# Optimization experiments

Hardware: AMD Instinct MI355X
Metric: run time of the kernel (lower is better)

## Reference

```python
import jax, jax.numpy as jnp
import numpy as np

TOP_K = 2


def setup_inputs() -> dict:
    key = jax.random.key(0)
    ks = jax.random.split(key, 4)
    T, E, D_IN, D_H, D_OUT = 8192, 8, 1024, 4096, 1024
    s_in = 1.0 / np.sqrt(D_IN)
    s_h = 1.0 / np.sqrt(D_H)
    return {
        "x": jax.random.normal(ks[0], (T, D_IN), dtype=jnp.float32),
        "Wg": jax.random.normal(ks[1], (D_IN, E), dtype=jnp.float32) * s_in,
        "bg": jnp.zeros((E,), dtype=jnp.float32),
        "W1": jax.random.normal(ks[2], (E, D_IN, D_H), dtype=jnp.float32) * s_in,
        "b1": jnp.zeros((E, D_H), dtype=jnp.float32),
        "W2": jax.random.normal(ks[3], (E, D_H, D_OUT), dtype=jnp.float32) * s_h,
        "b2": jnp.zeros((E, D_OUT), dtype=jnp.float32),
    }


def moe_forward(x, Wg, bg, W1, b1, W2, b2):
    # Top-k gate: logits [T,E] -> top-k -> softmax over the k selected logits,
    # scattered back into a dense [T,E] weight matrix (zeros elsewhere).
    logits = x @ Wg + bg                              # [T, E]
    topv, topi = jax.lax.top_k(logits, TOP_K)         # [T, k]
    topw = jax.nn.softmax(topv, axis=-1)              # [T, k]
    T, E = logits.shape
    weights = jnp.zeros((T, E), dtype=logits.dtype)
    rows = jnp.arange(T)[:, None]
    weights = weights.at[rows, topi].set(topw)        # dense gate weights [T, E]

    # Dense all-expert MLP (faithful to the naive torch module):
    h = jax.nn.relu(jnp.einsum("ti,eih->teh", x, W1) + b1[None])   # [T, E, H]
    expert_out = jnp.einsum("teh,eho->teo", h, W2) + b2[None]      # [T, E, O]

    # Top-k weighted sum over experts.
    return jnp.einsum("te,teo->to", weights, expert_out)           # [T, O]


def reference(x, Wg, bg, W1, b1, W2, b2):
    return moe_forward(x, Wg, bg, W1, b1, W2, b2)
```

## Files before the change

### kernel.cpp

```cpp
#include <hip/hip_runtime.h>
#include <hip/hip_bf16.h>
#include <stdint.h>

#define NTOK 8192
#define NE 8
#define DIN 1024
#define DH 4096
#define DOUT 1024
#define MAXMB 135

typedef __bf16 bf16;
typedef __bf16 bf16_8 __attribute__((ext_vector_type(8)));
typedef __bf16 bf16_4 __attribute__((ext_vector_type(4)));
typedef float f32_4 __attribute__((ext_vector_type(4)));

__device__ __forceinline__ void gl_lds16(const void* g, void* l) {
  __builtin_amdgcn_global_load_lds(
      (const __attribute__((address_space(1))) unsigned int*)g,
      (__attribute__((address_space(3))) unsigned int*)l, 16, 0, 0);
}

__global__ void gate_kernel(const float* __restrict__ x, const float* __restrict__ Wg,
                            const float* __restrict__ bg,
                            int* __restrict__ topi, float* __restrict__ topw) {
  int t = blockIdx.x * 4 + (threadIdx.x >> 6);
  int lane = threadIdx.x & 63;
  float acc[NE];
#pragma unroll
  for (int e = 0; e < NE; e++) acc[e] = 0.f;
  const float* xr = x + (size_t)t * DIN;
#pragma unroll
  for (int i = 0; i < DIN / 64; i++) {
    float xv = xr[lane + 64 * i];
    const float4* wr = (const float4*)(Wg + (size_t)(lane + 64 * i) * NE);
    float4 w0 = wr[0], w1 = wr[1];
    acc[0] += xv * w0.x; acc[1] += xv * w0.y; acc[2] += xv * w0.z; acc[3] += xv * w0.w;
    acc[4] += xv * w1.x; acc[5] += xv * w1.y; acc[6] += xv * w1.z; acc[7] += xv * w1.w;
  }
#pragma unroll
  for (int off = 32; off > 0; off >>= 1)
#pragma unroll
    for (int e = 0; e < NE; e++) acc[e] += __shfl_xor(acc[e], off, 64);
  if (lane == 0) {
    float lg[NE];
#pragma unroll
    for (int e = 0; e < NE; e++) lg[e] = acc[e] + bg[e];
    int i0 = 0; float v0 = lg[0];
#pragma unroll
    for (int e = 1; e < NE; e++) if (lg[e] > v0) { v0 = lg[e]; i0 = e; }
    int i1 = -1; float v1 = -3.0e38f;
#pragma unroll
    for (int e = 0; e < NE; e++) if (e != i0 && lg[e] > v1) { v1 = lg[e]; i1 = e; }
    float ex = expf(v1 - v0);
    float w0 = 1.f / (1.f + ex);
    float w1 = ex / (1.f + ex);
    topi[2 * t] = i0; topi[2 * t + 1] = i1;
    topw[2 * t] = w0; topw[2 * t + 1] = w1;
  }
}

__global__ void hist_kernel(const int* __restrict__ topi, int* __restrict__ counts,
                            int* __restrict__ pos) {
  __shared__ int bins[NE];
  __shared__ int base[NE];
  int tid = threadIdx.x;
  if (tid < NE) bins[tid] = 0;
  __syncthreads();
  int i = blockIdx.x * 256 + tid;
  int e = topi[i];
  int local = atomicAdd(&bins[e], 1);
  __syncthreads();
  if (tid < NE) base[tid] = atomicAdd(&counts[tid], bins[tid]);
  __syncthreads();
  pos[i] = base[e] + local;
}

__global__ void scan_kernel(const int* counts, int* offsets, int* mblk_off) {
  if (threadIdx.x == 0) {
    int s = 0, b = 0;
    for (int e = 0; e < NE; e++) {
      offsets[e] = s; mblk_off[e] = b;
      s += counts[e]; b += (counts[e] + 127) >> 7;
    }
    mblk_off[NE] = b;
  }
}

__global__ void pack_kernel(const int* __restrict__ topi,
                            const int* __restrict__ pos, const int* __restrict__ offsets,
                            int* __restrict__ tok_list, int* __restrict__ slot_of) {
  int i = blockIdx.x * 256 + threadIdx.x;
  int e = topi[i];
  int slot = offsets[e] + pos[i];
  tok_list[slot] = i >> 1;
  slot_of[i] = slot;
}

__global__ void cvtx_kernel(const float* __restrict__ x, bf16* __restrict__ xb) {
  size_t i = ((size_t)blockIdx.x * 256 + threadIdx.x) * 8;
  float4 a = *(const float4*)(x + i);
  float4 b = *(const float4*)(x + i + 4);
  bf16_8 o;
  o[0] = (bf16)a.x; o[1] = (bf16)a.y; o[2] = (bf16)a.z; o[3] = (bf16)a.w;
  o[4] = (bf16)b.x; o[5] = (bf16)b.y; o[6] = (bf16)b.z; o[7] = (bf16)b.w;
  *(bf16_8*)(xb + i) = o;
}

__global__ void tcvt_kernel(const float* __restrict__ src, bf16* __restrict__ dst,
                            int src_ld, long long src_es, int dst_ld, long long dst_es) {
  __shared__ bf16 tile[32][33];
  const float* s = src + blockIdx.z * src_es + (size_t)(blockIdx.x * 32) * src_ld + blockIdx.y * 32;
  bf16* d = dst + blockIdx.z * dst_es + (size_t)(blockIdx.y * 32) * dst_ld + blockIdx.x * 32;
  int tid = threadIdx.x;
  int r = tid >> 3, c4 = (tid & 7) * 4;
  float4 v = *(const float4*)(s + (size_t)r * src_ld + c4);
  tile[r][c4] = (bf16)v.x; tile[r][c4 + 1] = (bf16)v.y;
  tile[r][c4 + 2] = (bf16)v.z; tile[r][c4 + 3] = (bf16)v.w;
  __syncthreads();
  int n = tid >> 3, k4 = (tid & 7) * 4;
  bf16_4 o;
  o[0] = tile[k4][n]; o[1] = tile[k4 + 1][n]; o[2] = tile[k4 + 2][n]; o[3] = tile[k4 + 3][n];
  *(bf16_4*)(d + (size_t)n * dst_ld + k4) = o;
}



#define XCD_SWIZZLE()                                                     \
  int nbx = gridDim.x;                                                    \
  int orig = blockIdx.y * nbx + blockIdx.x;                               \
  int nwg = nbx * gridDim.y;             \
  int wgid = (orig & 7) * (nwg >> 3) + (orig >> 3);                       \
  int bxi = wgid % nbx;                                                   \
  int mb = wgid / nbx;

__global__ __launch_bounds__(256) void gemm1_kernel(
    const bf16* __restrict__ xb, const bf16* __restrict__ W1t,
    const float* __restrict__ b1, const int* __restrict__ counts,
    const int* __restrict__ offsets, const int* __restrict__ mblk_off,
    const int* __restrict__ tok_list,
    bf16* __restrict__ h, int hchunk, int hc0) {
  XCD_SWIZZLE();
  if (mb >= mblk_off[NE]) return;
  int e = 0;
  while (mb >= mblk_off[e + 1]) e++;
  int ne = counts[e];
  int m0 = (mb - mblk_off[e]) * 128;
  int off = offsets[e];
  int n0 = bxi * 128;

  __shared__ __align__(16) bf16 smem[6 * 128 * 32];
  bf16* ldsA = smem;
  bf16* ldsB = smem + 3 * 4096;

  int tid = threadIdx.x;
  int w = tid >> 6, lane = tid & 63;
  int scol = (((lane & 3) ^ (lane >> 3)) & 3) * 8;

  const bf16* gA[2]; const bf16* gB[2];
  bf16* lA[2]; bf16* lB[2];
#pragma unroll
  for (int j = 0; j < 2; j++) {
    int seg = w * 2 + j;
    int row = seg * 16 + (lane >> 2);
    int slot = off + m0 + row;
    int smax = off + ne - 1;
    if (slot > smax) slot = smax;
    int tok = tok_list[slot];
    gA[j] = xb + (size_t)tok * DIN + scol;
    lA[j] = ldsA + seg * 512;
    gB[j] = W1t + ((size_t)e * hchunk + n0 + row) * DIN + scol;
    lB[j] = ldsB + seg * 512;
  }

  f32_4 acc[4][4];
#pragma unroll
  for (int i = 0; i < 4; i++)
#pragma unroll
    for (int j = 0; j < 4; j++) acc[i][j] = (f32_4){0.f, 0.f, 0.f, 0.f};

  int wm = w & 1, wn = w >> 1;
  int lr = lane & 15, quad = lane >> 4;
  int rcol = ((quad ^ (lr >> 1)) & 3) * 8;

  auto compute = [&](int buf) {
    bf16_8 af[4], bfr[4];
#pragma unroll
    for (int mt = 0; mt < 4; mt++)
      af[mt] = *(const bf16_8*)(ldsA + buf * 4096 + (wm * 64 + mt * 16 + lr) * 32 + rcol);
#pragma unroll
    for (int nt = 0; nt < 4; nt++)
      bfr[nt] = *(const bf16_8*)(ldsB + buf * 4096 + (wn * 64 + nt * 16 + lr) * 32 + rcol);
#pragma unroll
    for (int mt = 0; mt < 4; mt++)
#pragma unroll
      for (int nt = 0; nt < 4; nt++)
        acc[mt][nt] = __builtin_amdgcn_mfma_f32_16x16x32_bf16(af[mt], bfr[nt], acc[mt][nt], 0, 0, 0);
  };

  const int nk = DIN / 32;
#pragma unroll
  for (int j = 0; j < 2; j++) { gl_lds16(gA[j], lA[j]); gl_lds16(gB[j], lB[j]); }
  gA[0] += 32; gA[1] += 32; gB[0] += 32; gB[1] += 32;
#pragma unroll
  for (int j = 0; j < 2; j++) { gl_lds16(gA[j], lA[j] + 4096); gl_lds16(gB[j], lB[j] + 4096); }
  gA[0] += 32; gA[1] += 32; gB[0] += 32; gB[1] += 32;

  int rb = 0, sb = 2;
  for (int kt = 0; kt < nk; kt++) {
    if (kt + 1 < nk) asm volatile("s_waitcnt vmcnt(4)" ::: "memory");
    else             asm volatile("s_waitcnt vmcnt(0)" ::: "memory");
    __builtin_amdgcn_s_barrier();
    __builtin_amdgcn_sched_barrier(0);
    if (kt + 2 < nk) {
#pragma unroll
      for (int j = 0; j < 2; j++) {
        gl_lds16(gA[j], lA[j] + sb * 4096);
        gl_lds16(gB[j], lB[j] + sb * 4096);
      }
      gA[0] += 32; gA[1] += 32; gB[0] += 32; gB[1] += 32;
    }
    __builtin_amdgcn_sched_barrier(0);
    compute(rb);
    rb = rb == 2 ? 0 : rb + 1;
    sb = sb == 2 ? 0 : sb + 1;
  }

  __syncthreads();
#pragma unroll
  for (int nt = 0; nt < 4; nt++) {
    int cloc = wn * 64 + nt * 16 + lr;
    float bias = b1[(size_t)e * DH + hc0 + n0 + cloc];
#pragma unroll
    for (int mt = 0; mt < 4; mt++) {
#pragma unroll
      for (int r2 = 0; r2 < 4; r2++) {
        int row = wm * 64 + mt * 16 + quad * 4 + r2;
        float v = acc[mt][nt][r2] + bias;
        v = v > 0.f ? v : 0.f;
        int byte = (row * 256 + cloc * 2) ^ (((row >> 2) & 7) << 4);
        *(bf16*)((char*)smem + byte) = (bf16)v;
      }
    }
  }
  __syncthreads();
#pragma unroll
  for (int p = 0; p < 8; p++) {
    int r = p * 16 + (tid >> 4);
    int b = tid & 15;
    if (m0 + r < ne) {
      int byte = (r * 256 + b * 16) ^ (((r >> 2) & 7) << 4);
      bf16_8 v = *(const bf16_8*)((char*)smem + byte);
      *(bf16_8*)(h + (size_t)(off + m0 + r) * hchunk + n0 + b * 8) = v;
    }
  }
}

__global__ __launch_bounds__(256) void gemm2_kernel(
    const bf16* __restrict__ h, const bf16* __restrict__ W2t,
    const int* __restrict__ counts, const int* __restrict__ offsets,
    const int* __restrict__ mblk_off,
    float* __restrict__ y, int hchunk, int accum) {
  XCD_SWIZZLE();
  if (mb >= mblk_off[NE]) return;
  int e = 0;
  while (mb >= mblk_off[e + 1]) e++;
  int ne = counts[e];
  int m0 = (mb - mblk_off[e]) * 128;
  int off = offsets[e];
  int n0 = bxi * 128;

  __shared__ __align__(16) bf16 smem[6 * 128 * 32];
  bf16* ldsA = smem;
  bf16* ldsB = smem + 3 * 4096;

  int tid = threadIdx.x;
  int w = tid >> 6, lane = tid & 63;
  int scol = (((lane & 3) ^ (lane >> 3)) & 3) * 8;

  const bf16* gA[2]; const bf16* gB[2];
  bf16* lA[2]; bf16* lB[2];
#pragma unroll
  for (int j = 0; j < 2; j++) {
    int seg = w * 2 + j;
    int row = seg * 16 + (lane >> 2);
    gA[j] = h + (size_t)(off + m0 + row) * hchunk + scol;
    lA[j] = ldsA + seg * 512;
    gB[j] = W2t + ((size_t)e * DOUT + n0 + row) * hchunk + scol;
    lB[j] = ldsB + seg * 512;
  }

  f32_4 acc[4][4];
#pragma unroll
  for (int i = 0; i < 4; i++)
#pragma unroll
    for (int j = 0; j < 4; j++) acc[i][j] = (f32_4){0.f, 0.f, 0.f, 0.f};

  int wm = w & 1, wn = w >> 1;
  int lr = lane & 15, quad = lane >> 4;
  int rcol = ((quad ^ (lr >> 1)) & 3) * 8;

  auto compute = [&](int buf) {
    bf16_8 af[4], bfr[4];
#pragma unroll
    for (int mt = 0; mt < 4; mt++)
      af[mt] = *(const bf16_8*)(ldsA + buf * 4096 + (wm * 64 + mt * 16 + lr) * 32 + rcol);
#pragma unroll
    for (int nt = 0; nt < 4; nt++)
      bfr[nt] = *(const bf16_8*)(ldsB + buf * 4096 + (wn * 64 + nt * 16 + lr) * 32 + rcol);
#pragma unroll
    for (int mt = 0; mt < 4; mt++)
#pragma unroll
      for (int nt = 0; nt < 4; nt++)
        acc[mt][nt] = __builtin_amdgcn_mfma_f32_16x16x32_bf16(af[mt], bfr[nt], acc[mt][nt], 0, 0, 0);
  };

  const int nk = hchunk / 32;
#pragma unroll
  for (int j = 0; j < 2; j++) { gl_lds16(gA[j], lA[j]); gl_lds16(gB[j], lB[j]); }
  gA[0] += 32; gA[1] += 32; gB[0] += 32; gB[1] += 32;
#pragma unroll
  for (int j = 0; j < 2; j++) { gl_lds16(gA[j], lA[j] + 4096); gl_lds16(gB[j], lB[j] + 4096); }
  gA[0] += 32; gA[1] += 32; gB[0] += 32; gB[1] += 32;

  int rb = 0, sb = 2;
  for (int kt = 0; kt < nk; kt++) {
    if (kt + 1 < nk) asm volatile("s_waitcnt vmcnt(4)" ::: "memory");
    else             asm volatile("s_waitcnt vmcnt(0)" ::: "memory");
    __builtin_amdgcn_s_barrier();
    __builtin_amdgcn_sched_barrier(0);
    if (kt + 2 < nk) {
#pragma unroll
      for (int j = 0; j < 2; j++) {
        gl_lds16(gA[j], lA[j] + sb * 4096);
        gl_lds16(gB[j], lB[j] + sb * 4096);
      }
      gA[0] += 32; gA[1] += 32; gB[0] += 32; gB[1] += 32;
    }
    __builtin_amdgcn_sched_barrier(0);
    compute(rb);
    rb = rb == 2 ? 0 : rb + 1;
    sb = sb == 2 ? 0 : sb + 1;
  }

#pragma unroll
  for (int mt = 0; mt < 4; mt++) {
#pragma unroll
    for (int r2 = 0; r2 < 4; r2++) {
      int row = wm * 64 + mt * 16 + quad * 4 + r2;
      if (m0 + row < ne) {
        float* yrow = y + (size_t)(off + m0 + row) * DOUT + n0;
#pragma unroll
        for (int nt = 0; nt < 4; nt++) {
          int c = wn * 64 + nt * 16 + lr;
          float v = acc[mt][nt][r2];
          if (accum) v += yrow[c];
          yrow[c] = v;
        }
      }
    }
  }
}

__global__ void combine_kernel(const int* __restrict__ topi, const float* __restrict__ topw,
                               const int* __restrict__ slot_of, const float* __restrict__ y,
                               const float* __restrict__ b2, float* __restrict__ out) {
  int t = blockIdx.x;
  int c = threadIdx.x * 4;
  int e0 = topi[2 * t], e1 = topi[2 * t + 1];
  float w0 = topw[2 * t], w1 = topw[2 * t + 1];
  int s0 = slot_of[2 * t], s1 = slot_of[2 * t + 1];
  float4 a = *(const float4*)(y + (size_t)s0 * DOUT + c);
  float4 b = *(const float4*)(y + (size_t)s1 * DOUT + c);
  float4 p = *(const float4*)(b2 + (size_t)e0 * DOUT + c);
  float4 q = *(const float4*)(b2 + (size_t)e1 * DOUT + c);
  float4 o;
  o.x = w0 * (a.x + p.x) + w1 * (b.x + q.x);
  o.y = w0 * (a.y + p.y) + w1 * (b.y + q.y);
  o.z = w0 * (a.z + p.z) + w1 * (b.z + q.z);
  o.w = w0 * (a.w + p.w) + w1 * (b.w + q.w);
  *(float4*)(out + (size_t)t * DOUT + c) = o;
}

extern "C" void kernel_launch(void* const* d_in, const int* in_sizes, int n_in,
                              void* d_out, int out_size, void* d_ws, size_t ws_size,
                              hipStream_t stream) {
  const float* x  = (const float*)d_in[0];
  const float* Wg = (const float*)d_in[1];
  const float* bg = (const float*)d_in[2];
  const float* W1 = (const float*)d_in[3];
  const float* b1 = (const float*)d_in[4];
  const float* W2 = (const float*)d_in[5];
  const float* b2 = (const float*)d_in[6];
  float* out = (float*)d_out;

  char* p = (char*)d_ws;
  int*   counts   = (int*)p;   p += 256;
  int*   offsets  = (int*)p;   p += 256;
  int*   mblk_off = (int*)p;   p += 256;
  int*   topi     = (int*)p;   p += 16384 * 4;
  float* topw     = (float*)p; p += 16384 * 4;
  int*   pos      = (int*)p;   p += 16384 * 4;
  int*   tok_list = (int*)p;   p += 16384 * 4;
  int*   slot_of  = (int*)p;   p += 16384 * 4;
  bf16*  xb       = (bf16*)p;  p += (size_t)NTOK * DIN * 2;
  float* y        = (float*)p; p += (size_t)16384 * DOUT * 4;

  size_t fixedBytes = (size_t)(p - (char*)d_ws);
  int hchunk = 4096;
  while (hchunk > 128 && fixedBytes + (size_t)hchunk * 65792 > ws_size) hchunk >>= 1;

  bf16* W1t  = (bf16*)p; p += (size_t)NE * hchunk * DIN * 2;
  bf16* W2t  = (bf16*)p; p += (size_t)NE * DOUT * hchunk * 2;
  bf16* hbuf = (bf16*)p; p += (size_t)(16384 + 128) * hchunk * 2;

  hipMemsetAsync(counts, 0, 32, stream);
  gate_kernel<<<NTOK / 4, 256, 0, stream>>>(x, Wg, bg, topi, topw);
  cvtx_kernel<<<(NTOK * DIN) / (8 * 256), 256, 0, stream>>>(x, xb);
  hist_kernel<<<64, 256, 0, stream>>>(topi, counts, pos);
  scan_kernel<<<1, 64, 0, stream>>>(counts, offsets, mblk_off);
  pack_kernel<<<64, 256, 0, stream>>>(topi, pos, offsets, tok_list, slot_of);

  int nchunks = DH / hchunk;
  for (int c = 0; c < nchunks; c++) {
    int hc0 = c * hchunk;
    tcvt_kernel<<<dim3(DIN / 32, hchunk / 32, NE), 256, 0, stream>>>(
        W1 + hc0, W1t, DH, (long long)DIN * DH, DIN, (long long)hchunk * DIN);
    tcvt_kernel<<<dim3(hchunk / 32, DOUT / 32, NE), 256, 0, stream>>>(
        W2 + (size_t)hc0 * DOUT, W2t, DOUT, (long long)DH * DOUT, hchunk, (long long)DOUT * hchunk);
    gemm1_kernel<<<dim3(hchunk / 128, MAXMB), 256, 0, stream>>>(
        xb, W1t, b1, counts, offsets, mblk_off, tok_list, hbuf, hchunk, hc0);
    gemm2_kernel<<<dim3(DOUT / 128, MAXMB), 256, 0, stream>>>(
        hbuf, W2t, counts, offsets, mblk_off, y, hchunk, c > 0 ? 1 : 0);
  }
  combine_kernel<<<NTOK, 256, 0, stream>>>(topi, topw, slot_of, y, b2, out);
}
```

Measured before the change: 769.7 us.

## Fuse combine into gemm2 via weighted atomics and fold bf16 cast into gate

The second GEMM now scales each row by its gate weight and atomically adds it into the output row of its token. A prefill kernel writes the weighted bias, so the intermediate y buffer and the combine kernel are removed. The x-to-bf16 conversion moves into the gate kernel, which already reads x. This removes a large fp32 round trip and one pass over x, at the cost of global float atomics and a nondeterministic summation order.

```diff
diff --git a/kernel.cpp b/kernel.cpp
--- a/kernel.cpp
+++ b/kernel.cpp
@@ -22,16 +22,19 @@
 
 __global__ void gate_kernel(const float* __restrict__ x, const float* __restrict__ Wg,
                             const float* __restrict__ bg,
-                            int* __restrict__ topi, float* __restrict__ topw) {
+                            int* __restrict__ topi, float* __restrict__ topw,
+                            bf16* __restrict__ xb) {
   int t = blockIdx.x * 4 + (threadIdx.x >> 6);
   int lane = threadIdx.x & 63;
   float acc[NE];
 #pragma unroll
   for (int e = 0; e < NE; e++) acc[e] = 0.f;
   const float* xr = x + (size_t)t * DIN;
+  bf16* xw = xb + (size_t)t * DIN;
 #pragma unroll
   for (int i = 0; i < DIN / 64; i++) {
     float xv = xr[lane + 64 * i];
+    xw[lane + 64 * i] = (bf16)xv;
     const float4* wr = (const float4*)(Wg + (size_t)(lane + 64 * i) * NE);
     float4 w0 = wr[0], w1 = wr[1];
     acc[0] += xv * w0.x; acc[1] += xv * w0.y; acc[2] += xv * w0.z; acc[3] += xv * w0.w;
@@ -88,22 +91,29 @@
 
 __global__ void pack_kernel(const int* __restrict__ topi,
                             const int* __restrict__ pos, const int* __restrict__ offsets,
-                            int* __restrict__ tok_list, int* __restrict__ slot_of) {
+                            const float* __restrict__ topw,
+                            int* __restrict__ tok_list, float* __restrict__ wt_list) {
   int i = blockIdx.x * 256 + threadIdx.x;
   int e = topi[i];
   int slot = offsets[e] + pos[i];
   tok_list[slot] = i >> 1;
-  slot_of[i] = slot;
-}
-
-__global__ void cvtx_kernel(const float* __restrict__ x, bf16* __restrict__ xb) {
-  size_t i = ((size_t)blockIdx.x * 256 + threadIdx.x) * 8;
-  float4 a = *(const float4*)(x + i);
-  float4 b = *(const float4*)(x + i + 4);
-  bf16_8 o;
-  o[0] = (bf16)a.x; o[1] = (bf16)a.y; o[2] = (bf16)a.z; o[3] = (bf16)a.w;
-  o[4] = (bf16)b.x; o[5] = (bf16)b.y; o[6] = (bf16)b.z; o[7] = (bf16)b.w;
-  *(bf16_8*)(xb + i) = o;
+  wt_list[slot] = topw[i];
+}
+
+__global__ void prefill_kernel(const int* __restrict__ topi, const float* __restrict__ topw,
+                               const float* __restrict__ b2, float* __restrict__ out) {
+  int t = blockIdx.x;
+  int c = threadIdx.x * 4;
+  int e0 = topi[2 * t], e1 = topi[2 * t + 1];
+  float w0 = topw[2 * t], w1 = topw[2 * t + 1];
+  float4 p = *(const float4*)(b2 + (size_t)e0 * DOUT + c);
+  float4 q = *(const float4*)(b2 + (size_t)e1 * DOUT + c);
+  float4 o;
+  o.x = w0 * p.x + w1 * q.x;
+  o.y = w0 * p.y + w1 * q.y;
+  o.z = w0 * p.z + w1 * q.z;
+  o.w = w0 * p.w + w1 * q.w;
+  *(float4*)(out + (size_t)t * DOUT + c) = o;
 }
 
 __global__ void tcvt_kernel(const float* __restrict__ src, bf16* __restrict__ dst,
@@ -125,21 +135,18 @@
 
 
 
-#define XCD_SWIZZLE()                                                     \
-  int nbx = gridDim.x;                                                    \
-  int orig = blockIdx.y * nbx + blockIdx.x;                               \
-  int nwg = nbx * gridDim.y;             \
-  int wgid = (orig & 7) * (nwg >> 3) + (orig >> 3);                       \
-  int bxi = wgid % nbx;                                                   \
-  int mb = wgid / nbx;
-
 __global__ __launch_bounds__(256) void gemm1_kernel(
     const bf16* __restrict__ xb, const bf16* __restrict__ W1t,
     const float* __restrict__ b1, const int* __restrict__ counts,
     const int* __restrict__ offsets, const int* __restrict__ mblk_off,
     const int* __restrict__ tok_list,
     bf16* __restrict__ h, int hchunk, int hc0) {
-  XCD_SWIZZLE();
+  int nbx = gridDim.x;
+  int orig = blockIdx.y * nbx + blockIdx.x;
+  int nwg = nbx * gridDim.y;
+  int wgid = (orig & 7) * (nwg >> 3) + (orig >> 3);
+  int bxi = wgid % nbx;
+  int mb = wgid / nbx;
   if (mb >= mblk_off[NE]) return;
   int e = 0;
   while (mb >= mblk_off[e + 1]) e++;
@@ -258,9 +265,15 @@
 __global__ __launch_bounds__(256) void gemm2_kernel(
     const bf16* __restrict__ h, const bf16* __restrict__ W2t,
     const int* __restrict__ counts, const int* __restrict__ offsets,
-    const int* __restrict__ mblk_off,
-    float* __restrict__ y, int hchunk, int accum) {
-  XCD_SWIZZLE();
+    const int* __restrict__ mblk_off, const int* __restrict__ tok_list,
+    const float* __restrict__ wt_list,
+    float* __restrict__ out, int hchunk) {
+  int nbx = gridDim.x;
+  int orig = blockIdx.y * nbx + blockIdx.x;
+  int nwg = nbx * gridDim.y;
+  int wgid = (orig & 7) * (nwg >> 3) + (orig >> 3);
+  int bxi = wgid % nbx;
+  int mb = wgid / nbx;
   if (mb >= mblk_off[NE]) return;
   int e = 0;
   while (mb >= mblk_off[e + 1]) e++;
@@ -348,37 +361,18 @@
     for (int r2 = 0; r2 < 4; r2++) {
       int row = wm * 64 + mt * 16 + quad * 4 + r2;
       if (m0 + row < ne) {
-        float* yrow = y + (size_t)(off + m0 + row) * DOUT + n0;
+        int slot = off + m0 + row;
+        int tok = tok_list[slot];
+        float wgt = wt_list[slot];
+        float* orow = out + (size_t)tok * DOUT + n0;
 #pragma unroll
         for (int nt = 0; nt < 4; nt++) {
           int c = wn * 64 + nt * 16 + lr;
-          float v = acc[mt][nt][r2];
-          if (accum) v += yrow[c];
-          yrow[c] = v;
+          atomicAdd(orow + c, wgt * acc[mt][nt][r2]);
         }
       }
     }
   }
-}
-
-__global__ void combine_kernel(const int* __restrict__ topi, const float* __restrict__ topw,
-                               const int* __restrict__ slot_of, const float* __restrict__ y,
-                               const float* __restrict__ b2, float* __restrict__ out) {
-  int t = blockIdx.x;
-  int c = threadIdx.x * 4;
-  int e0 = topi[2 * t], e1 = topi[2 * t + 1];
-  float w0 = topw[2 * t], w1 = topw[2 * t + 1];
-  int s0 = slot_of[2 * t], s1 = slot_of[2 * t + 1];
-  float4 a = *(const float4*)(y + (size_t)s0 * DOUT + c);
-  float4 b = *(const float4*)(y + (size_t)s1 * DOUT + c);
-  float4 p = *(const float4*)(b2 + (size_t)e0 * DOUT + c);
-  float4 q = *(const float4*)(b2 + (size_t)e1 * DOUT + c);
-  float4 o;
-  o.x = w0 * (a.x + p.x) + w1 * (b.x + q.x);
-  o.y = w0 * (a.y + p.y) + w1 * (b.y + q.y);
-  o.z = w0 * (a.z + p.z) + w1 * (b.z + q.z);
-  o.w = w0 * (a.w + p.w) + w1 * (b.w + q.w);
-  *(float4*)(out + (size_t)t * DOUT + c) = o;
 }
 
 extern "C" void kernel_launch(void* const* d_in, const int* in_sizes, int n_in,
@@ -401,9 +395,8 @@
   float* topw     = (float*)p; p += 16384 * 4;
   int*   pos      = (int*)p;   p += 16384 * 4;
   int*   tok_list = (int*)p;   p += 16384 * 4;
-  int*   slot_of  = (int*)p;   p += 16384 * 4;
+  float* wt_list  = (float*)p; p += 16384 * 4;
   bf16*  xb       = (bf16*)p;  p += (size_t)NTOK * DIN * 2;
-  float* y        = (float*)p; p += (size_t)16384 * DOUT * 4;
 
   size_t fixedBytes = (size_t)(p - (char*)d_ws);
   int hchunk = 4096;
@@ -414,11 +407,11 @@
   bf16* hbuf = (bf16*)p; p += (size_t)(16384 + 128) * hchunk * 2;
 
   hipMemsetAsync(counts, 0, 32, stream);
-  gate_kernel<<<NTOK / 4, 256, 0, stream>>>(x, Wg, bg, topi, topw);
-  cvtx_kernel<<<(NTOK * DIN) / (8 * 256), 256, 0, stream>>>(x, xb);
+  gate_kernel<<<NTOK / 4, 256, 0, stream>>>(x, Wg, bg, topi, topw, xb);
   hist_kernel<<<64, 256, 0, stream>>>(topi, counts, pos);
   scan_kernel<<<1, 64, 0, stream>>>(counts, offsets, mblk_off);
-  pack_kernel<<<64, 256, 0, stream>>>(topi, pos, offsets, tok_list, slot_of);
+  pack_kernel<<<64, 256, 0, stream>>>(topi, pos, offsets, topw, tok_list, wt_list);
+  prefill_kernel<<<NTOK, 256, 0, stream>>>(topi, topw, b2, out);
 
   int nchunks = DH / hchunk;
   for (int c = 0; c < nchunks; c++) {
@@ -430,7 +423,6 @@
     gemm1_kernel<<<dim3(hchunk / 128, MAXMB), 256, 0, stream>>>(
         xb, W1t, b1, counts, offsets, mblk_off, tok_list, hbuf, hchunk, hc0);
     gemm2_kernel<<<dim3(DOUT / 128, MAXMB), 256, 0, stream>>>(
-        hbuf, W2t, counts, offsets, mblk_off, y, hchunk, c > 0 ? 1 : 0);
-  }
-  combine_kernel<<<NTOK, 256, 0, stream>>>(topi, topw, slot_of, y, b2, out);
-}
+        hbuf, W2t, counts, offsets, mblk_off, tok_list, wt_list, out, hchunk);
+  }
+}
```

After: 776.4 us. Within noise of the previous version (+0.9%).
